# Performance work log

Measured on AMD Instinct MI355X. Metric: run time of the kernel, lower is better.

The kernel has to match this reference:

```python
import jax, jax.numpy as jnp
import numpy as np

N, E, F_IN, H, NC, NG = 50000, 800000, 256, 64, 4, 64

def setup_inputs() -> dict:
    key = jax.random.key(0)
    ks = jax.random.split(key, 12)
    inp = {
        'x': jax.random.normal(ks[0], (N, F_IN), dtype=jnp.float32),
        'edge_index': jax.random.randint(ks[1], (2, E), 0, N, dtype=jnp.int64),
        'batch': jnp.sort(jax.random.randint(ks[2], (N,), 0, NG, dtype=jnp.int64)),
        # GCNConv layer 1 and 2 (weight [in,out] + bias), Glorot-ish scale
        'W1': jax.random.normal(ks[3], (F_IN, H), dtype=jnp.float32) / np.sqrt(F_IN),
        'b1': jnp.zeros((H,), dtype=jnp.float32),
        'W2': jax.random.normal(ks[4], (H, H), dtype=jnp.float32) / np.sqrt(H),
        'b2': jnp.zeros((H,), dtype=jnp.float32),
        # MLP head
        'fc1_w': jax.random.normal(ks[5], (H, 128), dtype=jnp.float32) / np.sqrt(H),
        'fc1_b': jnp.zeros((128,), dtype=jnp.float32),
        'fc2_w': jax.random.normal(ks[6], (128, NC), dtype=jnp.float32) / np.sqrt(128),
        'fc2_b': jnp.zeros((NC,), dtype=jnp.float32),
    }
    return inp

def _gcn_conv(x, src, dst, W, b, n_nodes):
    # PyG GCNConv: add self-loops, symmetric norm D^-1/2 (A+I) D^-1/2, then X W + b
    h = x @ W  # [N, out]
    deg = jax.ops.segment_sum(jnp.ones_like(dst, dtype=h.dtype), dst, num_segments=n_nodes)
    dinv = jnp.where(deg > 0, jax.lax.rsqrt(deg), 0.0)
    norm = dinv[src] * dinv[dst]  # [E+N]
    msg = h[src] * norm[:, None]
    out = jax.ops.segment_sum(msg, dst, num_segments=n_nodes)
    return out + b

def reference(x, edge_index, batch, W1, b1, W2, b2, fc1_w, fc1_b, fc2_w, fc2_b):
    n = x.shape[0]
    loops = jnp.arange(n, dtype=edge_index.dtype)
    src = jnp.concatenate([edge_index[0], loops])
    dst = jnp.concatenate([edge_index[1], loops])
    h = jax.nn.relu(_gcn_conv(x, src, dst, W1, b1, n))
    h = jax.nn.relu(_gcn_conv(h, src, dst, W2, b2, n))
    # global_mean_pool over graph ids
    sums = jax.ops.segment_sum(h, batch, num_segments=NG)
    cnts = jax.ops.segment_sum(jnp.ones((n,), h.dtype), batch, num_segments=NG)
    pooled = sums / jnp.maximum(cnts, 1.0)[:, None]  # [NG, H]
    z = jax.nn.relu(pooled @ fc1_w + fc1_b)
    # dropout in eval mode = identity
    return z @ fc2_w + fc2_b  # [NG, NC]
```

## Files before the change

kernel.cpp:

```cpp
#include <hip/hip_runtime.h>


#define TPB 256
#define CHUNK_A 4096
#define BCAP 4608

typedef unsigned short bfu;
typedef __attribute__((ext_vector_type(8))) short s16x8;
typedef __attribute__((ext_vector_type(4))) float f32x4;

__device__ __forceinline__ float bf2f(bfu u) {
    union { unsigned u32; float f; } c; c.u32 = ((unsigned)u) << 16; return c.f;
}
__device__ __forceinline__ bfu f2bf(float f) {
    union { float f; unsigned u; } c; c.f = f;
    unsigned r = 0x7FFFu + ((c.u >> 16) & 1u);
    return (bfu)((c.u + r) >> 16);
}
__device__ __forceinline__ float blo(unsigned w) {
    union { unsigned u32; float f; } c; c.u32 = w << 16; return c.f;
}
__device__ __forceinline__ float bhi(unsigned w) {
    union { unsigned u32; float f; } c; c.u32 = w & 0xFFFF0000u; return c.f;
}


__global__ __launch_bounds__(TPB) void k_passA(const int* __restrict__ srcv,
                                               const int* __restrict__ dstv, int E,
                                               int* __restrict__ gcur,
                                               int* __restrict__ staged, int nbuck) {
    __shared__ int pk[CHUNK_A];
    __shared__ int hist[256];
    __shared__ int ebase[256];
    __shared__ int gbase[256];
    __shared__ int lcur[256];
    int t = threadIdx.x;
    int e0 = blockIdx.x * CHUNK_A;
    int e1 = e0 + CHUNK_A; if (e1 > E) e1 = E;

    hist[t] = 0; lcur[t] = 0;
    __syncthreads();
    for (int i = e0 + t; i < e1; i += TPB) atomicAdd(&hist[dstv[i] >> 8], 1);
    __syncthreads();
    int v = hist[t];
    ebase[t] = v;
    __syncthreads();
    for (int off = 1; off < 256; off <<= 1) {
        int u = (t >= off) ? ebase[t - off] : 0;
        __syncthreads();
        ebase[t] += u;
        __syncthreads();
    }
    ebase[t] -= v;
    if (t < nbuck && v > 0) gbase[t] = t * BCAP + atomicAdd(&gcur[t], v);
    __syncthreads();
    for (int i = e0 + t; i < e1; i += TPB) {
        int d = dstv[i];
        int s = srcv[i];
        int b = d >> 8;
        int r = atomicAdd(&lcur[b], 1);
        pk[ebase[b] + r] = (s << 8) | (d & 255);
    }
    __syncthreads();
    int wave = t >> 6, lane = t & 63;
    for (int b = wave; b < nbuck; b += 4) {
        int c = hist[b];
        int lb = ebase[b];
        int gb = gbase[b];
        for (int j = lane; j < c; j += 64) staged[gb + j] = pk[lb + j];
    }
}


__global__ __launch_bounds__(TPB) void k_passB(const int* __restrict__ staged,
                                               const int* __restrict__ gcur,
                                               int* __restrict__ csr_off,
                                               int* __restrict__ csr_src,
                                               float* __restrict__ dinv,
                                               int n, int nbuck) {
    __shared__ int pk[BCAP];
    __shared__ int soff[256];
    __shared__ int hist[256];
    __shared__ int nbase[256];
    __shared__ int cur[256];
    int b = blockIdx.x;
    int n0 = b << 8;
    int n1 = n0 + 256; if (n1 > n) n1 = n;
    int cnt = gcur[b];
    int t = threadIdx.x;

    int cv = (t < nbuck) ? gcur[t] : 0;
    soff[t] = cv;
    hist[t] = 0; cur[t] = 0;
    __syncthreads();
    for (int off = 1; off < 256; off <<= 1) {
        int u = (t >= off) ? soff[t - off] : 0;
        __syncthreads();
        soff[t] += u;
        __syncthreads();
    }
    int base = soff[b] - cnt;

    for (int i = t; i < cnt; i += TPB) pk[i] = staged[b * BCAP + i];
    __syncthreads();
    for (int i = t; i < cnt; i += TPB) atomicAdd(&hist[pk[i] & 255], 1);
    __syncthreads();
    int v = hist[t];
    nbase[t] = v;
    __syncthreads();
    for (int off = 1; off < 256; off <<= 1) {
        int u = (t >= off) ? nbase[t - off] : 0;
        __syncthreads();
        nbase[t] += u;
        __syncthreads();
    }
    nbase[t] -= v;
    if (n0 + t < n1) {
        csr_off[n0 + t] = base + nbase[t];
        dinv[n0 + t] = rsqrtf((float)(v + 1));
    }
    if (b == nbuck - 1 && t == 0) csr_off[n] = base + cnt;
    __syncthreads();
    for (int i = t; i < cnt; i += TPB) {
        int p = pk[i];
        int dloc = p & 255;
        int r = atomicAdd(&cur[dloc], 1);
        csr_src[base + nbase[dloc] + r] = p >> 8;
    }
}


__device__ __forceinline__ int swz(int rc, int k) {
    return rc * 64 + (k ^ ((rc & 7) << 3));
}

__global__ __launch_bounds__(TPB) void k_gemm1(const float* __restrict__ A,
                                               const float* __restrict__ W,
                                               const float* __restrict__ dinv,
                                               bfu* __restrict__ C, int n) {
    const int K = 256;
    __shared__ __align__(16) ushort Ah[128 * 64];
    __shared__ __align__(16) ushort Bh[64 * 64];

    const int t = threadIdx.x;
    const int wave = t >> 6, lane = t & 63;
    const int rbase = blockIdx.x * 128;

    f32x4 acc[2][4];
#pragma unroll
    for (int i = 0; i < 2; i++)
#pragma unroll
        for (int j = 0; j < 4; j++) acc[i][j] = {0.f, 0.f, 0.f, 0.f};

    for (int kc = 0; kc < K; kc += 64) {
        {
            int c = t & 63;
            int kg = (t >> 6) << 4;
#pragma unroll
            for (int q = 0; q < 4; q++) {
                ushort4 h4;
#pragma unroll
                for (int j = 0; j < 4; j++) {
                    ((bfu*)&h4)[j] = f2bf(W[(size_t)(kc + kg + q * 4 + j) * 64 + c]);
                }
                *(ushort4*)&Bh[swz(c, kg + q * 4)] = h4;
            }
        }
        {
#pragma unroll
            for (int q = 0; q < 8; q++) {
                int idx = q * 256 + t;
                int row = idx >> 4;
                int k4 = (idx & 15) << 2;
                int r = rbase + row;
                float4 xv = make_float4(0.f, 0.f, 0.f, 0.f);
                if (r < n) xv = *(const float4*)&A[(size_t)r * K + kc + k4];
                ushort4 h4;
                ((bfu*)&h4)[0] = f2bf(xv.x);
                ((bfu*)&h4)[1] = f2bf(xv.y);
                ((bfu*)&h4)[2] = f2bf(xv.z);
                ((bfu*)&h4)[3] = f2bf(xv.w);
                *(ushort4*)&Ah[swz(row, k4)] = h4;
            }
        }
        __syncthreads();

        const int rl = lane & 15;
        const int kg8 = (lane >> 4) << 3;
#pragma unroll
        for (int ks = 0; ks < 2; ks++) {
            int k0 = ks * 32 + kg8;
            s16x8 a_h[2], b_h[4];
#pragma unroll
            for (int rt = 0; rt < 2; rt++) {
                int row = wave * 32 + rt * 16 + rl;
                a_h[rt] = *(const s16x8*)&Ah[swz(row, k0)];
            }
#pragma unroll
            for (int ct = 0; ct < 4; ct++) {
                int cc = ct * 16 + rl;
                b_h[ct] = *(const s16x8*)&Bh[swz(cc, k0)];
            }
#pragma unroll
            for (int rt = 0; rt < 2; rt++)
#pragma unroll
                for (int ct = 0; ct < 4; ct++) {
                    acc[rt][ct] = __builtin_amdgcn_mfma_f32_16x16x32_bf16(
                        a_h[rt], b_h[ct], acc[rt][ct], 0, 0, 0);
                }
        }
        __syncthreads();
    }

    const int rl = lane & 15;
    const int rq = (lane >> 4) << 2;
#pragma unroll
    for (int rt = 0; rt < 2; rt++) {
#pragma unroll
        for (int reg = 0; reg < 4; reg++) {
            int r = rbase + wave * 32 + rt * 16 + rq + reg;
            if (r < n) {
                float d = dinv[r];
#pragma unroll
                for (int ct = 0; ct < 4; ct++) {
                    C[(size_t)r * 64 + ct * 16 + rl] = f2bf(acc[rt][ct][reg] * d);
                }
            }
        }
    }
}


__device__ __forceinline__ void acc_u4(float* acc, uint4 q) {
    acc[0] += blo(q.x); acc[1] += bhi(q.x);
    acc[2] += blo(q.y); acc[3] += bhi(q.y);
    acc[4] += blo(q.z); acc[5] += bhi(q.z);
    acc[6] += blo(q.w); acc[7] += bhi(q.w);
}

template <bool FUSE>
__global__ __launch_bounds__(TPB) void k_agg(const bfu* __restrict__ hs,
                                             const int* __restrict__ csr_off,
                                             const int* __restrict__ csr_src,
                                             const float* __restrict__ dinv,
                                             const float* __restrict__ bias,
                                             const float* __restrict__ W2,
                                             bfu* __restrict__ out, int n) {
    __shared__ float rowbuf[4][64];
    int wv = threadIdx.x >> 6;
    int node = blockIdx.x * 4 + wv;
    int lane = threadIdx.x & 63;
    int g = lane >> 3;
    int c = lane & 7;
    if (node >= n) return;
    int p0 = csr_off[node];
    int p1 = csr_off[node + 1];
    int deg = p1 - p0;
    float d = dinv[node];

    uint4 selfv = *(const uint4*)(hs + (size_t)node * 64 + c * 8);

    float acc[8];
#pragma unroll
    for (int j = 0; j < 8; j++) acc[j] = 0.f;

    for (int base = 0; base < deg; base += 16) {
        int rem = deg - base;
        int li0 = p0 + base + g;
        if (rem > 8) {
            int li1 = li0 + 8;
            int idx0 = csr_src[li0];
            int idx1 = csr_src[li1 < p1 ? li1 : p0];
            bool v1 = (8 + g) < rem;
            uint4 q0 = *(const uint4*)(hs + (size_t)idx0 * 64 + c * 8);
            uint4 q1 = *(const uint4*)(hs + (size_t)(v1 ? idx1 : node) * 64 + c * 8);
            if (!v1) q1 = make_uint4(0u, 0u, 0u, 0u);
            acc_u4(acc, q0);
            acc_u4(acc, q1);
        } else {
            bool v0 = g < rem;
            int idx0 = csr_src[li0 < p1 ? li0 : p0];
            uint4 q0 = *(const uint4*)(hs + (size_t)(v0 ? idx0 : node) * 64 + c * 8);
            if (!v0) q0 = make_uint4(0u, 0u, 0u, 0u);
            acc_u4(acc, q0);
        }
    }

#pragma unroll
    for (int j = 0; j < 8; j++) {
        acc[j] += __shfl_xor(acc[j], 8);
        acc[j] += __shfl_xor(acc[j], 16);
        acc[j] += __shfl_xor(acc[j], 32);
    }
    acc_u4(acc, selfv);

    float4 b0 = *(const float4*)&bias[c * 8];
    float4 b1 = *(const float4*)&bias[c * 8 + 4];
    float v[8];
    v[0] = fmaxf(d * acc[0] + b0.x, 0.f);
    v[1] = fmaxf(d * acc[1] + b0.y, 0.f);
    v[2] = fmaxf(d * acc[2] + b0.z, 0.f);
    v[3] = fmaxf(d * acc[3] + b0.w, 0.f);
    v[4] = fmaxf(d * acc[4] + b1.x, 0.f);
    v[5] = fmaxf(d * acc[5] + b1.y, 0.f);
    v[6] = fmaxf(d * acc[6] + b1.z, 0.f);
    v[7] = fmaxf(d * acc[7] + b1.w, 0.f);

    if (!FUSE) {
        if (g == 0) {
            uint4 o;
            o.x = (unsigned)f2bf(v[0]) | ((unsigned)f2bf(v[1]) << 16);
            o.y = (unsigned)f2bf(v[2]) | ((unsigned)f2bf(v[3]) << 16);
            o.z = (unsigned)f2bf(v[4]) | ((unsigned)f2bf(v[5]) << 16);
            o.w = (unsigned)f2bf(v[6]) | ((unsigned)f2bf(v[7]) << 16);
            *(uint4*)(out + (size_t)node * 64 + c * 8) = o;
        }
    } else {
        if (g == 0) {
            *(float4*)&rowbuf[wv][c * 8]     = make_float4(v[0], v[1], v[2], v[3]);
            *(float4*)&rowbuf[wv][c * 8 + 4] = make_float4(v[4], v[5], v[6], v[7]);
        }
        __builtin_amdgcn_wave_barrier();
        float a = 0.f;
#pragma unroll 16
        for (int k = 0; k < 64; k++) a += rowbuf[wv][k] * W2[k * 64 + lane];
        out[(size_t)node * 64 + lane] = f2bf(d * a);
    }
}


__global__ __launch_bounds__(TPB) void k_pool(const bfu* __restrict__ h,
                                              const int* __restrict__ batch, int n,
                                              float* __restrict__ gsum,
                                              int* __restrict__ gcnt) {
    const int CH = 16;
    int wid = blockIdx.x * 4 + (threadIdx.x >> 6);
    int lane = threadIdx.x & 63;
    int i0 = wid * CH;
    if (i0 >= n) return;
    int i1 = i0 + CH; if (i1 > n) i1 = n;
    int g0 = batch[i0];
    int g1 = batch[i1 - 1];
    if (g0 == g1) {
        float acc = 0.f;
#pragma unroll
        for (int i = 0; i < CH; i++) {
            int idx = i0 + i;
            if (idx < i1) acc += bf2f(h[(size_t)idx * 64 + lane]);
        }
        atomicAdd(&gsum[g0 * 64 + lane], acc);
        if (lane == 0) atomicAdd(&gcnt[g0], i1 - i0);
    } else {
        int cur = g0;
        float acc = 0.f;
        int cnt = 0;
        for (int i = i0; i < i1; i++) {
            int g = batch[i];
            if (g != cur) {
                atomicAdd(&gsum[cur * 64 + lane], acc);
                if (lane == 0) atomicAdd(&gcnt[cur], cnt);
                acc = 0.f; cnt = 0; cur = g;
            }
            acc += bf2f(h[(size_t)i * 64 + lane]);
            cnt++;
        }
        atomicAdd(&gsum[cur * 64 + lane], acc);
        if (lane == 0) atomicAdd(&gcnt[cur], cnt);
    }
}


__global__ __launch_bounds__(TPB) void k_head1(const float* __restrict__ gsum,
                                               const int* __restrict__ gcnt,
                                               const float* __restrict__ fc1w,
                                               const float* __restrict__ fc1b,
                                               float* __restrict__ z) {
    int t = threadIdx.x;
    int g = blockIdx.x * 2 + (t >> 7);
    int o = t & 127;
    int c = gcnt[g]; if (c < 1) c = 1;
    float inv = 1.0f / (float)c;
    float a = fc1b[o];
#pragma unroll 16
    for (int j = 0; j < 64; j++) {
        float pj = gsum[g * 64 + j] * inv;
        a += pj * fc1w[j * 128 + o];
    }
    z[g * 128 + o] = fmaxf(a, 0.f);
}


__global__ __launch_bounds__(TPB) void k_head2(const float* __restrict__ z,
                                               const float* __restrict__ fc2w,
                                               const float* __restrict__ fc2b,
                                               float* __restrict__ out) {
    int t = threadIdx.x;
    int g = t >> 2, c = t & 3;
    float a = fc2b[c];
#pragma unroll 16
    for (int o = 0; o < 128; o++) a += z[g * 128 + o] * fc2w[o * 4 + c];
    out[t] = a;
}


extern "C" void kernel_launch(void* const* d_in, const int* in_sizes, int n_in,
                              void* d_out, int out_size, void* d_ws, size_t ws_size,
                              hipStream_t stream) {
    const float* x    = (const float*)d_in[0];
    const int*   ei   = (const int*)d_in[1];
    const int*   batch= (const int*)d_in[2];
    const float* W1   = (const float*)d_in[3];
    const float* b1   = (const float*)d_in[4];
    const float* W2   = (const float*)d_in[5];
    const float* b2   = (const float*)d_in[6];
    const float* fc1w = (const float*)d_in[7];
    const float* fc1b = (const float*)d_in[8];
    const float* fc2w = (const float*)d_in[9];
    const float* fc2b = (const float*)d_in[10];

    const int n = in_sizes[2];
    const int E = in_sizes[1] / 2;
    const int* srcv = ei;
    const int* dstv = ei + E;
    const int nbuck = (n + 255) >> 8;

    char* w = (char*)d_ws;
    int*   gcur   = (int*)w;            w += 256 * 4;
    int*   gcnt   = (int*)w;            w += 64 * 4;
    float* gsum   = (float*)w;          w += 64 * 64 * 4;
    size_t zbytes = (size_t)w - (size_t)d_ws;
    int*   csr_off= (int*)w;            w += (size_t)(n + 1) * 4;
    float* dinv   = (float*)w;          w += (size_t)n * 4;
    int*   csr_src= (int*)w;            w += (size_t)E * 4;
    int*   staged = (int*)w;            w += (size_t)nbuck * BCAP * 4;
    float* zbuf   = (float*)w;          w += 64 * 128 * 4;
    w = (char*)(((size_t)w + 255) & ~(size_t)255);
    bfu* hs = (bfu*)w;                  w += (size_t)n * 64 * 2;
    w = (char*)(((size_t)w + 255) & ~(size_t)255);
    bfu* hb = (bfu*)w;                  w += (size_t)n * 64 * 2;

    hipMemsetAsync(d_ws, 0, zbytes, stream);

    int gA = (E + CHUNK_A - 1) / CHUNK_A;
    k_passA<<<gA, TPB, 0, stream>>>(srcv, dstv, E, gcur, staged, nbuck);
    k_passB<<<nbuck, TPB, 0, stream>>>(staged, gcur, csr_off, csr_src, dinv, n, nbuck);

    int gRows = (n + 127) / 128;
    int gNode = (n + 3) / 4;
    k_gemm1<<<gRows, TPB, 0, stream>>>(x, W1, dinv, hs, n);
    k_agg<true><<<gNode, TPB, 0, stream>>>(hs, csr_off, csr_src, dinv, b1, W2, hb, n);
    k_agg<false><<<gNode, TPB, 0, stream>>>(hb, csr_off, csr_src, dinv, b2, nullptr, hs, n);

    int nwaves16 = (n + 15) / 16;
    k_pool<<<(nwaves16 + 3) / 4, TPB, 0, stream>>>(hs, batch, n, gsum, gcnt);
    k_head1<<<32, TPB, 0, stream>>>(gsum, gcnt, fc1w, fc1b, zbuf);
    k_head2<<<1, TPB, 0, stream>>>(zbuf, fc2w, fc2b, (float*)d_out);
}
```

Baseline: 256.9 us.

## Stage full W1 in LDS once and stream A rows directly into MFMA registers

The first GEMM now converts all of W1 (256x64) to bf16 in shared memory once per block with a wider swizzle. Each wave loads its 16 rows of x straight from global memory into MFMA operand registers, so the A tile no longer goes through LDS and the per-K-chunk barriers are gone. Block rows drop from 128 to 64, which doubles the grid. The trade-off is that every block re-converts the whole W1, and A loads are 32-byte strided per lane rather than coalesced tile loads.

```diff
diff --git a/kernel.cpp b/kernel.cpp
--- a/kernel.cpp
+++ b/kernel.cpp
@@ -130,8 +130,8 @@
 }
 
 
-__device__ __forceinline__ int swz(int rc, int k) {
-    return rc * 64 + (k ^ ((rc & 7) << 3));
+__device__ __forceinline__ int swzW(int c, int k) {
+    return c * 256 + (k ^ ((c & 15) << 3));
 }
 
 __global__ __launch_bounds__(TPB) void k_gemm1(const float* __restrict__ A,
@@ -139,92 +139,68 @@
                                                const float* __restrict__ dinv,
                                                bfu* __restrict__ C, int n) {
     const int K = 256;
-    __shared__ __align__(16) ushort Ah[128 * 64];
-    __shared__ __align__(16) ushort Bh[64 * 64];
+    __shared__ __align__(16) ushort Bh[64 * 256];
 
     const int t = threadIdx.x;
     const int wave = t >> 6, lane = t & 63;
-    const int rbase = blockIdx.x * 128;
-
-    f32x4 acc[2][4];
-#pragma unroll
-    for (int i = 0; i < 2; i++)
-#pragma unroll
-        for (int j = 0; j < 4; j++) acc[i][j] = {0.f, 0.f, 0.f, 0.f};
-
-    for (int kc = 0; kc < K; kc += 64) {
-        {
-            int c = t & 63;
-            int kg = (t >> 6) << 4;
-#pragma unroll
-            for (int q = 0; q < 4; q++) {
-                ushort4 h4;
-#pragma unroll
-                for (int j = 0; j < 4; j++) {
-                    ((bfu*)&h4)[j] = f2bf(W[(size_t)(kc + kg + q * 4 + j) * 64 + c]);
-                }
-                *(ushort4*)&Bh[swz(c, kg + q * 4)] = h4;
-            }
-        }
-        {
-#pragma unroll
-            for (int q = 0; q < 8; q++) {
-                int idx = q * 256 + t;
-                int row = idx >> 4;
-                int k4 = (idx & 15) << 2;
-                int r = rbase + row;
-                float4 xv = make_float4(0.f, 0.f, 0.f, 0.f);
-                if (r < n) xv = *(const float4*)&A[(size_t)r * K + kc + k4];
-                ushort4 h4;
-                ((bfu*)&h4)[0] = f2bf(xv.x);
-                ((bfu*)&h4)[1] = f2bf(xv.y);
-                ((bfu*)&h4)[2] = f2bf(xv.z);
-                ((bfu*)&h4)[3] = f2bf(xv.w);
-                *(ushort4*)&Ah[swz(row, k4)] = h4;
-            }
-        }
-        __syncthreads();
-
-        const int rl = lane & 15;
-        const int kg8 = (lane >> 4) << 3;
-#pragma unroll
-        for (int ks = 0; ks < 2; ks++) {
-            int k0 = ks * 32 + kg8;
-            s16x8 a_h[2], b_h[4];
-#pragma unroll
-            for (int rt = 0; rt < 2; rt++) {
-                int row = wave * 32 + rt * 16 + rl;
-                a_h[rt] = *(const s16x8*)&Ah[swz(row, k0)];
-            }
+    const int rbase = blockIdx.x * 64;
+
+    {
+        int c = t & 63;
+        int kg = (t >> 6) << 6;
+#pragma unroll
+        for (int q = 0; q < 8; q++) {
+            int k8 = kg + q * 8;
+            ushort4 h0, h1;
+#pragma unroll
+            for (int j = 0; j < 4; j++) ((bfu*)&h0)[j] = f2bf(W[(size_t)(k8 + j) * 64 + c]);
+#pragma unroll
+            for (int j = 0; j < 4; j++) ((bfu*)&h1)[j] = f2bf(W[(size_t)(k8 + 4 + j) * 64 + c]);
+            *(ushort4*)&Bh[swzW(c, k8)]     = h0;
+            *(ushort4*)&Bh[swzW(c, k8) + 4] = h1;
+        }
+    }
+    __syncthreads();
+
+    const int rl = lane & 15;
+    const int kg8 = (lane >> 4) << 3;
+    int r0 = rbase + wave * 16 + rl;
+    const float* arow = A + (size_t)(r0 < n ? r0 : (n - 1)) * K;
+
+    f32x4 acc[4];
+#pragma unroll
+    for (int j = 0; j < 4; j++) acc[j] = {0.f, 0.f, 0.f, 0.f};
+
+#pragma unroll
+    for (int ks = 0; ks < 8; ks++) {
+        int k0 = ks * 32 + kg8;
+        float4 xa = *(const float4*)(arow + k0);
+        float4 xb = *(const float4*)(arow + k0 + 4);
+        s16x8 af;
+        ((bfu*)&af)[0] = f2bf(xa.x);
+        ((bfu*)&af)[1] = f2bf(xa.y);
+        ((bfu*)&af)[2] = f2bf(xa.z);
+        ((bfu*)&af)[3] = f2bf(xa.w);
+        ((bfu*)&af)[4] = f2bf(xb.x);
+        ((bfu*)&af)[5] = f2bf(xb.y);
+        ((bfu*)&af)[6] = f2bf(xb.z);
+        ((bfu*)&af)[7] = f2bf(xb.w);
+#pragma unroll
+        for (int ct = 0; ct < 4; ct++) {
+            s16x8 bf = *(const s16x8*)&Bh[swzW(ct * 16 + rl, k0)];
+            acc[ct] = __builtin_amdgcn_mfma_f32_16x16x32_bf16(af, bf, acc[ct], 0, 0, 0);
+        }
+    }
+
+    const int rq = (lane >> 4) << 2;
+#pragma unroll
+    for (int reg = 0; reg < 4; reg++) {
+        int r = rbase + wave * 16 + rq + reg;
+        if (r < n) {
+            float d = dinv[r];
 #pragma unroll
             for (int ct = 0; ct < 4; ct++) {
-                int cc = ct * 16 + rl;
-                b_h[ct] = *(const s16x8*)&Bh[swz(cc, k0)];
-            }
-#pragma unroll
-            for (int rt = 0; rt < 2; rt++)
-#pragma unroll
-                for (int ct = 0; ct < 4; ct++) {
-                    acc[rt][ct] = __builtin_amdgcn_mfma_f32_16x16x32_bf16(
-                        a_h[rt], b_h[ct], acc[rt][ct], 0, 0, 0);
-                }
-        }
-        __syncthreads();
-    }
-
-    const int rl = lane & 15;
-    const int rq = (lane >> 4) << 2;
-#pragma unroll
-    for (int rt = 0; rt < 2; rt++) {
-#pragma unroll
-        for (int reg = 0; reg < 4; reg++) {
-            int r = rbase + wave * 32 + rt * 16 + rq + reg;
-            if (r < n) {
-                float d = dinv[r];
-#pragma unroll
-                for (int ct = 0; ct < 4; ct++) {
-                    C[(size_t)r * 64 + ct * 16 + rl] = f2bf(acc[rt][ct][reg] * d);
-                }
+                C[(size_t)r * 64 + ct * 16 + rl] = f2bf(acc[ct][reg] * d);
             }
         }
     }
@@ -445,7 +421,7 @@
     k_passA<<<gA, TPB, 0, stream>>>(srcv, dstv, E, gcur, staged, nbuck);
     k_passB<<<nbuck, TPB, 0, stream>>>(staged, gcur, csr_off, csr_src, dinv, n, nbuck);
 
-    int gRows = (n + 127) / 128;
+    int gRows = (n + 63) / 64;
     int gNode = (n + 3) / 4;
     k_gemm1<<<gRows, TPB, 0, stream>>>(x, W1, dinv, hs, n);
     k_agg<true><<<gNode, TPB, 0, stream>>>(hs, csr_off, csr_src, dinv, b1, W2, hb, n);
```

New measurement: 235.6 us. 8.3% less time.
